# Kernel tuning notes

Measured on AMD Instinct MI355X. Metric: run time of the kernel, lower is better.

Reference implementation:

```python
import jax, jax.numpy as jnp
import numpy as np

TAU = 12.5        # from init_kwargs
THRESHOLD = 0.5   # from init_kwargs


def setup_inputs() -> dict:
    key = jax.random.key(0)
    stimulus = jax.random.normal(key, (4, 4096, 2048), dtype=jnp.float32)
    return {
        "stimulus": stimulus,
        "a": jnp.float32(0.7),   # nn.Parameter init 0.7
        "b": jnp.float32(0.8),   # nn.Parameter init 0.8
        "dt": jnp.float32(1.0),  # nn.Parameter init 1.0
        "n_steps": 8,
    }


def reference(stimulus, a, b, dt, n_steps):
    # Stimulus conditioning (matches torch forward exactly)
    stim_scale = jnp.clip(jnp.max(jnp.abs(stimulus), axis=-1, keepdims=True), 1e-6, None)
    stimulus_normed = stimulus / stim_scale
    threshold_gate = jax.nn.sigmoid((jnp.abs(stimulus) - THRESHOLD) * 10.0)
    I = stimulus_normed * (0.1 + 0.9 * threshold_gate)

    v = jnp.zeros_like(stimulus)
    w = jnp.zeros_like(stimulus)

    # IMEX FHN update loop (use_imex=True path). Note: the torch code computes an
    # intermediate w_new that is never used; only w_next (built from v_next) matters.
    alpha = dt / TAU
    denom = 1.0 + alpha * b
    for _ in range(n_steps):  # n_steps is a static Python int -> unrolled under jit
        dv_explicit = v - (v * v * v) / 3.0 - w + I
        v_next = v + dt * dv_explicit
        w_next = (w + alpha * (v_next + a)) / denom
        v = jnp.clip(v_next, -3.0, 3.0)
        w = jnp.clip(w_next, -3.0, 3.0)

    response = v * stim_scale
    return response, v
```

## Files before the change

kernel.cpp:

```cpp
#include <hip/hip_runtime.h>
#include <math.h>


#define ROWLEN 2048
#define BLOCK  256
#define EPT    8
#define F4PT   (EPT / 4)

__global__ __launch_bounds__(BLOCK)
void fhn_kernel(const float* __restrict__ stim,
                const float* __restrict__ a_p,
                const float* __restrict__ b_p,
                const float* __restrict__ dt_p,
                const int*   __restrict__ nsteps_p,
                float* __restrict__ out,
                long long n_elem)
{
    const long long row = blockIdx.x;
    const float* __restrict__ srow = stim + row * ROWLEN;
    float* __restrict__ rrow = out + row * ROWLEN;
    float* __restrict__ vrow = out + n_elem + row * ROWLEN;

    const int tid = threadIdx.x;

    float s[EPT];
    #pragma unroll
    for (int i = 0; i < F4PT; ++i) {
        float4 f = reinterpret_cast<const float4*>(srow)[tid + i * BLOCK];
        s[4*i+0] = f.x; s[4*i+1] = f.y; s[4*i+2] = f.z; s[4*i+3] = f.w;
    }

    float m = 0.0f;
    #pragma unroll
    for (int e = 0; e < EPT; ++e) m = fmaxf(m, fabsf(s[e]));
    #pragma unroll
    for (int off = 32; off > 0; off >>= 1)
        m = fmaxf(m, __shfl_down(m, off, 64));
    __shared__ float smax[BLOCK / 64];
    if ((tid & 63) == 0) smax[tid >> 6] = m;
    __syncthreads();
    m = fmaxf(fmaxf(smax[0], smax[1]), fmaxf(smax[2], smax[3]));

    const float scale     = fmaxf(m, 1e-6f);
    const float inv_scale = 1.0f / scale;

    const float a  = *a_p;
    const float b  = *b_p;
    const float dt = *dt_p;
    const int   n_steps = *nsteps_p;
    const float alpha     = dt / 12.5f;
    const float inv_denom = 1.0f / (1.0f + alpha * b);

    float I[EPT], v[EPT], w[EPT];
    #pragma unroll
    for (int e = 0; e < EPT; ++e) {
        const float as   = fabsf(s[e]);
        const float gate = 1.0f / (1.0f + __expf(-(as - 0.5f) * 10.0f));
        I[e] = s[e] * inv_scale * (0.1f + 0.9f * gate);
        v[e] = 0.0f;
        w[e] = 0.0f;
    }

    for (int n = 0; n < n_steps; ++n) {
        #pragma unroll
        for (int e = 0; e < EPT; ++e) {
            const float ve = v[e];
            const float dv = ve - ve * ve * ve * (1.0f / 3.0f) - w[e] + I[e];
            const float vn = ve + dt * dv;
            const float wn = (w[e] + alpha * (vn + a)) * inv_denom;
            v[e] = fminf(fmaxf(vn, -3.0f), 3.0f);
            w[e] = fminf(fmaxf(wn, -3.0f), 3.0f);
        }
    }

    #pragma unroll
    for (int i = 0; i < F4PT; ++i) {
        float4 r, vv;
        r.x  = v[4*i+0] * scale; r.y  = v[4*i+1] * scale;
        r.z  = v[4*i+2] * scale; r.w  = v[4*i+3] * scale;
        vv.x = v[4*i+0];         vv.y = v[4*i+1];
        vv.z = v[4*i+2];         vv.w = v[4*i+3];
        reinterpret_cast<float4*>(rrow)[tid + i * BLOCK] = r;
        reinterpret_cast<float4*>(vrow)[tid + i * BLOCK] = vv;
    }
}

extern "C" void kernel_launch(void* const* d_in, const int* in_sizes, int n_in,
                              void* d_out, int out_size, void* d_ws, size_t ws_size,
                              hipStream_t stream) {
    const float* stim = (const float*)d_in[0];
    const float* a_p  = (const float*)d_in[1];
    const float* b_p  = (const float*)d_in[2];
    const float* dt_p = (const float*)d_in[3];
    const int*   n_p  = (const int*)d_in[4];
    float* out = (float*)d_out;

    const long long n_elem = (long long)in_sizes[0];
    const int rows = (int)(n_elem / ROWLEN);

    fhn_kernel<<<rows, BLOCK, 0, stream>>>(stim, a_p, b_p, dt_p, n_p, out, n_elem);
}
```

Baseline: 367.2 us.

## Use one wavefront per row in a persistent loop with next-row prefetch

```diff
diff --git a/kernel.cpp b/kernel.cpp
--- a/kernel.cpp
+++ b/kernel.cpp
@@ -4,8 +4,10 @@
 
 #define ROWLEN 2048
 #define BLOCK  256
-#define EPT    8
-#define F4PT   (EPT / 4)
+#define F4PL   8
+#define EPL    32
+
+typedef float vfloat4 __attribute__((ext_vector_type(4)));
 
 __global__ __launch_bounds__(BLOCK)
 void fhn_kernel(const float* __restrict__ stim,
@@ -14,35 +16,13 @@
                 const float* __restrict__ dt_p,
                 const int*   __restrict__ nsteps_p,
                 float* __restrict__ out,
-                long long n_elem)
+                long long n_elem, int rows)
 {
-    const long long row = blockIdx.x;
-    const float* __restrict__ srow = stim + row * ROWLEN;
-    float* __restrict__ rrow = out + row * ROWLEN;
-    float* __restrict__ vrow = out + n_elem + row * ROWLEN;
+    const int lane    = threadIdx.x & 63;
+    const int wave_id = (blockIdx.x * BLOCK + threadIdx.x) >> 6;
+    const int nwaves  = (gridDim.x * BLOCK) >> 6;
 
-    const int tid = threadIdx.x;
-
-    float s[EPT];
-    #pragma unroll
-    for (int i = 0; i < F4PT; ++i) {
-        float4 f = reinterpret_cast<const float4*>(srow)[tid + i * BLOCK];
-        s[4*i+0] = f.x; s[4*i+1] = f.y; s[4*i+2] = f.z; s[4*i+3] = f.w;
-    }
-
-    float m = 0.0f;
-    #pragma unroll
-    for (int e = 0; e < EPT; ++e) m = fmaxf(m, fabsf(s[e]));
-    #pragma unroll
-    for (int off = 32; off > 0; off >>= 1)
-        m = fmaxf(m, __shfl_down(m, off, 64));
-    __shared__ float smax[BLOCK / 64];
-    if ((tid & 63) == 0) smax[tid >> 6] = m;
-    __syncthreads();
-    m = fmaxf(fmaxf(smax[0], smax[1]), fmaxf(smax[2], smax[3]));
-
-    const float scale     = fmaxf(m, 1e-6f);
-    const float inv_scale = 1.0f / scale;
+    if (wave_id >= rows) return;
 
     const float a  = *a_p;
     const float b  = *b_p;
@@ -51,37 +31,83 @@
     const float alpha     = dt / 12.5f;
     const float inv_denom = 1.0f / (1.0f + alpha * b);
 
-    float I[EPT], v[EPT], w[EPT];
-    #pragma unroll
-    for (int e = 0; e < EPT; ++e) {
-        const float as   = fabsf(s[e]);
-        const float gate = 1.0f / (1.0f + __expf(-(as - 0.5f) * 10.0f));
-        I[e] = s[e] * inv_scale * (0.1f + 0.9f * gate);
-        v[e] = 0.0f;
-        w[e] = 0.0f;
+    vfloat4 cur[F4PL], nxt[F4PL];
+
+    {
+        const vfloat4* src =
+            reinterpret_cast<const vfloat4*>(stim + (long long)wave_id * ROWLEN);
+        #pragma unroll
+        for (int k = 0; k < F4PL; ++k)
+            cur[k] = src[lane + 64 * k];
+        #pragma unroll
+        for (int k = 0; k < F4PL; ++k)
+            nxt[k] = (vfloat4)(0.0f);
     }
 
-    for (int n = 0; n < n_steps; ++n) {
+    for (int row = wave_id; row < rows; row += nwaves) {
+        const int nrow = row + nwaves;
+        if (nrow < rows) {
+            const vfloat4* src =
+                reinterpret_cast<const vfloat4*>(stim + (long long)nrow * ROWLEN);
+            #pragma unroll
+            for (int k = 0; k < F4PL; ++k)
+                nxt[k] = src[lane + 64 * k];
+        }
+
+        float m = 0.0f;
         #pragma unroll
-        for (int e = 0; e < EPT; ++e) {
-            const float ve = v[e];
-            const float dv = ve - ve * ve * ve * (1.0f / 3.0f) - w[e] + I[e];
-            const float vn = ve + dt * dv;
-            const float wn = (w[e] + alpha * (vn + a)) * inv_denom;
-            v[e] = fminf(fmaxf(vn, -3.0f), 3.0f);
-            w[e] = fminf(fmaxf(wn, -3.0f), 3.0f);
+        for (int k = 0; k < F4PL; ++k) {
+            m = fmaxf(m, fmaxf(fmaxf(fabsf(cur[k].x), fabsf(cur[k].y)),
+                               fmaxf(fabsf(cur[k].z), fabsf(cur[k].w))));
         }
-    }
+        #pragma unroll
+        for (int off = 32; off > 0; off >>= 1)
+            m = fmaxf(m, __shfl_xor(m, off, 64));
 
-    #pragma unroll
-    for (int i = 0; i < F4PT; ++i) {
-        float4 r, vv;
-        r.x  = v[4*i+0] * scale; r.y  = v[4*i+1] * scale;
-        r.z  = v[4*i+2] * scale; r.w  = v[4*i+3] * scale;
-        vv.x = v[4*i+0];         vv.y = v[4*i+1];
-        vv.z = v[4*i+2];         vv.w = v[4*i+3];
-        reinterpret_cast<float4*>(rrow)[tid + i * BLOCK] = r;
-        reinterpret_cast<float4*>(vrow)[tid + i * BLOCK] = vv;
+        const float scale     = fmaxf(m, 1e-6f);
+        const float inv_scale = 1.0f / scale;
+
+        float I[EPL], v[EPL], w[EPL];
+        #pragma unroll
+        for (int k = 0; k < F4PL; ++k) {
+            #pragma unroll
+            for (int j = 0; j < 4; ++j) {
+                const float s    = cur[k][j];
+                const float gate = 1.0f / (1.0f + __expf(-(fabsf(s) - 0.5f) * 10.0f));
+                I[4 * k + j] = s * inv_scale * (0.1f + 0.9f * gate);
+                v[4 * k + j] = 0.0f;
+                w[4 * k + j] = 0.0f;
+            }
+        }
+
+        for (int n = 0; n < n_steps; ++n) {
+            #pragma unroll
+            for (int e = 0; e < EPL; ++e) {
+                const float ve = v[e];
+                const float dv = ve - ve * ve * ve * (1.0f / 3.0f) - w[e] + I[e];
+                const float vn = ve + dt * dv;
+                const float wn = (w[e] + alpha * (vn + a)) * inv_denom;
+                v[e] = fminf(fmaxf(vn, -3.0f), 3.0f);
+                w[e] = fminf(fmaxf(wn, -3.0f), 3.0f);
+            }
+        }
+
+        vfloat4* rrow = reinterpret_cast<vfloat4*>(out + (long long)row * ROWLEN);
+        vfloat4* vrow = reinterpret_cast<vfloat4*>(out + n_elem + (long long)row * ROWLEN);
+        #pragma unroll
+        for (int k = 0; k < F4PL; ++k) {
+            vfloat4 r, vv;
+            r.x  = v[4 * k + 0] * scale; r.y  = v[4 * k + 1] * scale;
+            r.z  = v[4 * k + 2] * scale; r.w  = v[4 * k + 3] * scale;
+            vv.x = v[4 * k + 0];         vv.y = v[4 * k + 1];
+            vv.z = v[4 * k + 2];         vv.w = v[4 * k + 3];
+            __builtin_nontemporal_store(r,  rrow + lane + 64 * k);
+            __builtin_nontemporal_store(vv, vrow + lane + 64 * k);
+        }
+
+        #pragma unroll
+        for (int k = 0; k < F4PL; ++k)
+            cur[k] = nxt[k];
     }
 }
 
@@ -97,6 +123,12 @@
 
     const long long n_elem = (long long)in_sizes[0];
     const int rows = (int)(n_elem / ROWLEN);
+    if (rows <= 0) return;
 
-    fhn_kernel<<<rows, BLOCK, 0, stream>>>(stim, a_p, b_p, dt_p, n_p, out, n_elem);
+    int blocks = (rows + 3) / 4;
+    if (blocks > 1024) blocks = 1024;
+    if (blocks < 1)    blocks = 1;
+
+    fhn_kernel<<<blocks, BLOCK, 0, stream>>>(stim, a_p, b_p, dt_p, n_p,
+                                             out, n_elem, rows);
 }
```

New measurement: 382.3 us. 4.1% more time.
